# Kernel tuning notes

Measured on AMD Instinct MI355X. Metric: run time of the kernel, lower is better.

## Reference

```python
import jax, jax.numpy as jnp
import numpy as np

N, MAX_NB, H, L, V, B, M = 16384, 15, 512, 128, 1024, 256, 65536


def setup_inputs() -> dict:
    key = jax.random.key(0)
    ks = jax.random.split(key, 32)
    s = 0.02  # param init scale
    inp = {
        'x_ids': jax.random.randint(ks[0], (N,), 0, V, dtype=jnp.int32),
        'contexts': jax.random.randint(ks[1], (N,), 0, B, dtype=jnp.int32),
        'nei_idx': jax.random.randint(ks[2], (N, MAX_NB), 0, M, dtype=jnp.int32),
        'nei_mask': jax.random.randint(ks[3], (N, MAX_NB), 0, 2, dtype=jnp.int32),
        'o_idx': jax.random.randint(ks[4], (N, MAX_NB), 0, M, dtype=jnp.int32),
        'o_mask': jax.random.randint(ks[5], (N, MAX_NB), 0, 2, dtype=jnp.int32),
        'H_msg': jax.random.normal(ks[6], (M, H), jnp.float32),
        'x_tree_vecs': jax.random.normal(ks[7], (B, L), jnp.float32),
        'embedding': jax.random.normal(ks[8], (V, H), jnp.float32) * s,
        'Wz_w': jax.random.normal(ks[9], (H, 2 * H), jnp.float32) * s,
        'Wz_b': jnp.zeros((H,), jnp.float32),
        'Wr_w': jax.random.normal(ks[10], (H, H), jnp.float32) * s,
        'Wr_b': jnp.zeros((H,), jnp.float32),
        'Ur_w': jax.random.normal(ks[11], (H, H), jnp.float32) * s,
        'Wh_w': jax.random.normal(ks[12], (H, 2 * H), jnp.float32) * s,
        'Wh_b': jnp.zeros((H,), jnp.float32),
        'W_w': jax.random.normal(ks[13], (H, H + L), jnp.float32) * s,
        'W_b': jnp.zeros((H,), jnp.float32),
        'Wo_w': jax.random.normal(ks[14], (V, H), jnp.float32) * s,
        'Wo_b': jnp.zeros((V,), jnp.float32),
        'Ui_w': jax.random.normal(ks[15], (H, 2 * H), jnp.float32) * s,
        'Ui_b': jnp.zeros((H,), jnp.float32),
        'U_w': jax.random.normal(ks[16], (H, H + L), jnp.float32) * s,
        'U_b': jnp.zeros((H,), jnp.float32),
        'Uo_w': jax.random.normal(ks[17], (1, H), jnp.float32) * s,
        'Uo_b': jnp.zeros((1,), jnp.float32),
    }
    return inp


def _gru(x, h_nei, Wz_w, Wz_b, Wr_w, Wr_b, Ur_w, Wh_w, Wh_b):
    # x: [N,H], h_nei: [N,MAX_NB,H]
    sum_h = h_nei.sum(axis=1)
    z = jax.nn.sigmoid(jnp.concatenate([x, sum_h], axis=1) @ Wz_w.T + Wz_b)
    r1 = (x @ Wr_w.T + Wr_b)[:, None, :]          # [N,1,H]
    r2 = jnp.einsum('nkh,gh->nkg', h_nei, Ur_w)   # U_r(h_nei), no bias
    r = jax.nn.sigmoid(r1 + r2)
    sum_gated = (r * h_nei).sum(axis=1)
    pre_h = jnp.tanh(jnp.concatenate([x, sum_gated], axis=1) @ Wh_w.T + Wh_b)
    return (1.0 - z) * sum_h + z * pre_h


def reference(x_ids, contexts, nei_idx, nei_mask, o_idx, o_mask, H_msg,
              x_tree_vecs, embedding, Wz_w, Wz_b, Wr_w, Wr_b, Ur_w,
              Wh_w, Wh_b, W_w, W_b, Wo_w, Wo_b, Ui_w, Ui_b, U_w, U_b,
              Uo_w, Uo_b):
    x = embedding[x_ids]                                   # [N,H]
    h_nei = H_msg[nei_idx] * nei_mask[..., None].astype(H_msg.dtype)  # [N,NB,H]
    o_nei = H_msg[o_idx] * o_mask[..., None].astype(H_msg.dtype)
    new_h = _gru(x, h_nei, Wz_w, Wz_b, Wr_w, Wr_b, Ur_w, Wh_w, Wh_b)
    cur_o = o_nei.sum(axis=1)                              # [N,H]
    ctx = x_tree_vecs[contexts]                            # [N,L]
    # word prediction: aggregate(new_h, contexts, x_tree_vecs, 'word')
    w_hid = jax.nn.relu(jnp.concatenate([new_h, ctx], axis=1) @ W_w.T + W_b)
    word_scores = w_hid @ Wo_w.T + Wo_b                    # [N,V]
    # stop prediction: U_i(cat(x, cur_o)) -> aggregate(..., 'stop')
    stop_h = jax.nn.relu(jnp.concatenate([x, cur_o], axis=1) @ Ui_w.T + Ui_b)
    s_hid = jax.nn.relu(jnp.concatenate([stop_h, ctx], axis=1) @ U_w.T + U_b)
    stop_scores = s_hid @ Uo_w.T + Uo_b                    # [N,1]
    return jnp.concatenate([word_scores, stop_scores], axis=1)  # [N,V+1]
```

## Files before the change

kernel.cpp:

```cpp
#include <hip/hip_runtime.h>
#include <hip/hip_bf16.h>

typedef unsigned short u16;
typedef unsigned int u32;
typedef __attribute__((ext_vector_type(8))) short s8v;
typedef __attribute__((ext_vector_type(4))) float f4v;

#define HDIM 512
#define NNODE 16384
#define NB 15

__device__ __forceinline__ u16 f2bu(float x) {
  union { float f; u32 i; } v; v.f = x;
  u32 r = v.i + 0x7FFFu + ((v.i >> 16) & 1u);
  return (u16)(r >> 16);
}
__device__ __forceinline__ float bu2f(u16 u) {
  union { u32 i; float f; } v; v.i = ((u32)u) << 16;
  return v.f;
}
__device__ __forceinline__ u32 pk(float a, float b) {
  return (u32)f2bu(a) | ((u32)f2bu(b) << 16);
}
__device__ __forceinline__ float sigm(float x) {
  return __builtin_amdgcn_rcpf(1.f + __expf(-x));
}
__device__ __forceinline__ void gl16(const void* g, void* l) {
  __builtin_amdgcn_global_load_lds(
      (const __attribute__((address_space(1))) u32*)g,
      (__attribute__((address_space(3))) u32*)l, 16, 0, 0);
}
template<int N> __device__ __forceinline__ void wait_vm() {
  if constexpr (N == 0) asm volatile("s_waitcnt vmcnt(0)" ::: "memory");
  else if constexpr (N == 2) asm volatile("s_waitcnt vmcnt(2)" ::: "memory");
  else asm volatile("s_waitcnt vmcnt(4)" ::: "memory");
}

__global__ __launch_bounds__(256) void k_cvt_all(
    const float* Wz_w, const float* Wr_w, const float* Wh_w, const float* Ui_w,
    const float* Ur_w, const float* W_w, const float* U_w, const float* Wo_w,
    const float* emb, const float* xtree,
    const float* Wz_b, const float* Wr_b, const float* Wh_b, const float* Ui_b,
    const float* W_b, const float* U_b,
    u16* wcat, u16* wz_h, u16* wh_h, u16* ui_h, u16* ur, u16* w_n, u16* u_n,
    u16* ccat, u16* wo, u16* emb_bf, u16* xt_bf, float* ebias, float* cbias) {
  int seg = blockIdx.y;
  const float* src = nullptr; u16* dst = nullptr;
  const float* fsrc = nullptr; float* fdst = nullptr;
  int R = 0, Cs = 0, c0 = 0, C = 0, fn = 0;
  switch (seg) {
    case 0:  src = Wz_w; dst = wcat;              R = 512;  Cs = 1024; c0 = 0;   C = 512; break;
    case 1:  src = Wr_w; dst = wcat + 512 * 512;  R = 512;  Cs = 512;  c0 = 0;   C = 512; break;
    case 2:  src = Wh_w; dst = wcat + 1024 * 512; R = 512;  Cs = 1024; c0 = 0;   C = 512; break;
    case 3:  src = Ui_w; dst = wcat + 1536 * 512; R = 512;  Cs = 1024; c0 = 0;   C = 512; break;
    case 4:  src = Wz_w; dst = wz_h;              R = 512;  Cs = 1024; c0 = 512; C = 512; break;
    case 5:  src = Wh_w; dst = wh_h;              R = 512;  Cs = 1024; c0 = 512; C = 512; break;
    case 6:  src = Ui_w; dst = ui_h;              R = 512;  Cs = 1024; c0 = 512; C = 512; break;
    case 7:  src = Ur_w; dst = ur;                R = 512;  Cs = 512;  c0 = 0;   C = 512; break;
    case 8:  src = W_w;  dst = w_n;               R = 512;  Cs = 640;  c0 = 0;   C = 512; break;
    case 9:  src = U_w;  dst = u_n;               R = 512;  Cs = 640;  c0 = 0;   C = 512; break;
    case 10: src = W_w;  dst = ccat;              R = 512;  Cs = 640;  c0 = 512; C = 128; break;
    case 11: src = U_w;  dst = ccat + 512 * 128;  R = 512;  Cs = 640;  c0 = 512; C = 128; break;
    case 12: src = Wo_w; dst = wo;                R = 1024; Cs = 512;  c0 = 0;   C = 512; break;
    case 13: src = emb;  dst = emb_bf;            R = 1024; Cs = 512;  c0 = 0;   C = 512; break;
    case 14: src = xtree; dst = xt_bf;            R = 256;  Cs = 128;  c0 = 0;   C = 128; break;
    case 15: fsrc = Wz_b; fdst = ebias;        fn = 512; break;
    case 16: fsrc = Wr_b; fdst = ebias + 512;  fn = 512; break;
    case 17: fsrc = Wh_b; fdst = ebias + 1024; fn = 512; break;
    case 18: fsrc = Ui_b; fdst = ebias + 1536; fn = 512; break;
    case 19: fsrc = W_b;  fdst = cbias;        fn = 512; break;
    case 20: fsrc = U_b;  fdst = cbias + 512;  fn = 512; break;
  }
  int i = blockIdx.x * 256 + threadIdx.x;
  if (fdst) { if (i < fn) fdst[i] = fsrc[i]; return; }
  int e0 = i * 8;
  if (e0 >= R * C) return;
  int r = e0 / C, c = e0 - r * C;
  const float* s = src + (size_t)r * Cs + c0 + c;
  float4 a = *reinterpret_cast<const float4*>(s);
  float4 b = *reinterpret_cast<const float4*>(s + 4);
  uint4 o = {pk(a.x, a.y), pk(a.z, a.w), pk(b.x, b.y), pk(b.z, b.w)};
  *reinterpret_cast<uint4*>(&dst[e0]) = o;
}

__global__ void k_cvtH(const float* __restrict__ src, u16* __restrict__ HR) {
  size_t i = ((size_t)blockIdx.x * 256 + threadIdx.x) * 8;
  size_t m = i >> 9, c = i & 511;
  float4 a = *reinterpret_cast<const float4*>(src + i);
  float4 b = *reinterpret_cast<const float4*>(src + i + 4);
  uint4 o = {pk(a.x, a.y), pk(a.z, a.w), pk(b.x, b.y), pk(b.z, b.w)};
  *reinterpret_cast<uint4*>(&HR[m * 1024 + c]) = o;
}

struct GP {
  const u16* A; const u16* B; int K; int lda;
  const float* gadd; int ldg; const int* gidx;
  const float* bias; const u16* shb;
  float* outf; u16* outh; int ldo;
};

template<int EP>
__device__ __forceinline__ void epi(int row, int col, float v, const GP& g) {
  if constexpr (EP == 0) {
    g.outf[(size_t)row * g.ldo + col] = v + (g.bias ? g.bias[col] : 0.f);
  } else if constexpr (EP == 3) {
    float pre = v + g.gadd[(size_t)g.gidx[row] * g.ldg + col];
    g.outh[(size_t)row * g.ldo + col] = f2bu(pre > 0.f ? pre : 0.f);
  } else {
    g.outh[(size_t)row * g.ldo + col] = f2bu(v);
  }
}

template<int EP, int KV>
__device__ void gemm_core(const GP& g, u16* AsB, u16* BsB) {
  const int tid = threadIdx.x, lane = tid & 63, w = tid >> 6;
  const int wm = (w >> 2) * 64, wn = (w & 3) * 32;
  const int nx = gridDim.x;
  int orig = blockIdx.y * nx + blockIdx.x;
  int q = (nx * gridDim.y) >> 3;
  int tile = (orig & 7) * q + (orig >> 3);
  const int n0 = (tile % nx) * 128, m0 = (tile / nx) * 128;

  const int sr = tid >> 2, sc = (tid & 3) ^ (sr & 3);
  const u16* gA = g.A + (size_t)(m0 + sr) * g.lda + sc * 8;
  const u16* gB = g.B + (size_t)(n0 + sr) * KV + sc * 8;
  const int ls = tid * 8;

  f4v acc[4][2];
  f4v z4 = {0.f, 0.f, 0.f, 0.f};
#pragma unroll
  for (int a = 0; a < 4; a++) { acc[a][0] = z4; acc[a][1] = z4; }

  constexpr int T = KV / 32;
  auto STAGE = [&](int t) {
    int buf = (t & 3) * 4096;
    gl16(gA + t * 32, AsB + buf + ls);
    gl16(gB + t * 32, BsB + buf + ls);
  };
  STAGE(0); STAGE(1); STAGE(2);

#pragma unroll
  for (int t = 0; t < T; t++) {
    if (t < T - 2) wait_vm<4>();
    else if (t == T - 2) wait_vm<2>();
    else wait_vm<0>();
    __builtin_amdgcn_s_barrier();
    asm volatile("" ::: "memory");
    if (t + 3 < T) STAGE(t + 3);
    const u16* as = AsB + (t & 3) * 4096;
    const u16* bs = BsB + (t & 3) * 4096;
    s8v af[4], bf[2];
    int cc = lane >> 4;
#pragma unroll
    for (int i = 0; i < 4; i++) {
      int R = wm + i * 16 + (lane & 15);
      af[i] = *reinterpret_cast<const s8v*>(&as[R * 32 + (cc ^ (R & 3)) * 8]);
    }
#pragma unroll
    for (int i = 0; i < 2; i++) {
      int C = wn + i * 16 + (lane & 15);
      bf[i] = *reinterpret_cast<const s8v*>(&bs[C * 32 + (cc ^ (C & 3)) * 8]);
    }
#pragma unroll
    for (int mi = 0; mi < 4; mi++)
#pragma unroll
      for (int ni = 0; ni < 2; ni++)
        acc[mi][ni] = __builtin_amdgcn_mfma_f32_16x16x32_bf16(
            af[mi], bf[ni], acc[mi][ni], 0, 0, 0);
  }
#pragma unroll
  for (int mi = 0; mi < 4; mi++)
#pragma unroll
    for (int ni = 0; ni < 2; ni++)
#pragma unroll
      for (int r = 0; r < 4; r++) {
        int row = m0 + wm + mi * 16 + (lane >> 4) * 4 + r;
        int col = n0 + wn + ni * 16 + (lane & 15);
        epi<EP>(row, col, acc[mi][ni][r], g);
      }
}

template<int EP, int KV>
__global__ __launch_bounds__(512, 4) void k_gemm(GP g) {
  __shared__ u16 As[4 * 4096], Bs[4 * 4096];
  gemm_core<EP, KV>(g, As, Bs);
}

template<int EPa, int EPb, int KV>
__global__ __launch_bounds__(512, 4) void k_pair(GP a, GP b) {
  __shared__ u16 As[4 * 4096], Bs[4 * 4096];
  if (blockIdx.z == 0) gemm_core<EPa, KV>(a, As, Bs);
  else gemm_core<EPb, KV>(b, As, Bs);
}

__global__ __launch_bounds__(512, 4) void k_zn(
    const u16* __restrict__ sumh, const u16* __restrict__ sg,
    const u16* __restrict__ Wz, const u16* __restrict__ Wh,
    const float* __restrict__ E_z, const float* __restrict__ E_h, int ldg,
    const int* __restrict__ gidx, u16* __restrict__ newh) {
  __shared__ u16 As1[128 * 64], Bs1[128 * 64], As2[128 * 64], Bs2[128 * 64];
  const int tid = threadIdx.x, lane = tid & 63, w = tid >> 6;
  const int wm = (w >> 2) * 64, wn = (w & 3) * 32;
  const int nx = gridDim.x;
  int orig = blockIdx.y * nx + blockIdx.x;
  int q = (nx * gridDim.y) >> 3;
  int tile = (orig & 7) * q + (orig >> 3);
  const int n0 = (tile % nx) * 128, m0 = (tile / nx) * 128;

  const u16 *gA1[2], *gA2[2], *gB1[2], *gB2[2]; int ls[2];
#pragma unroll
  for (int i = 0; i < 2; i++) {
    int slot = tid + i * 512;
    int r = slot >> 3, c = (slot & 7) ^ (r & 7);
    gA1[i] = sumh + (size_t)(m0 + r) * HDIM + c * 8;
    gA2[i] = sg + (size_t)(m0 + r) * HDIM + c * 8;
    gB1[i] = Wz + (size_t)(n0 + r) * HDIM + c * 8;
    gB2[i] = Wh + (size_t)(n0 + r) * HDIM + c * 8;
    ls[i] = slot * 8;
  }

  f4v az[4][2], ah[4][2];
  f4v z4 = {0.f, 0.f, 0.f, 0.f};
#pragma unroll
  for (int a = 0; a < 4; a++) {
    az[a][0] = z4; az[a][1] = z4; ah[a][0] = z4; ah[a][1] = z4;
  }

  for (int k0 = 0; k0 < HDIM; k0 += 64) {
    __syncthreads();
#pragma unroll
    for (int i = 0; i < 2; i++) gl16(gA1[i] + k0, As1 + ls[i]);
#pragma unroll
    for (int i = 0; i < 2; i++) gl16(gB1[i] + k0, Bs1 + ls[i]);
#pragma unroll
    for (int i = 0; i < 2; i++) gl16(gA2[i] + k0, As2 + ls[i]);
#pragma unroll
    for (int i = 0; i < 2; i++) gl16(gB2[i] + k0, Bs2 + ls[i]);
    __syncthreads();
#pragma unroll
    for (int ks = 0; ks < 2; ks++) {
      int cc = ks * 4 + (lane >> 4);
      {
        s8v af[4], bf[2];
#pragma unroll
        for (int i = 0; i < 4; i++) {
          int R = wm + i * 16 + (lane & 15);
          af[i] = *reinterpret_cast<const s8v*>(&As1[R * 64 + (cc ^ (R & 7)) * 8]);
        }
#pragma unroll
        for (int i = 0; i < 2; i++) {
          int C = wn + i * 16 + (lane & 15);
          bf[i] = *reinterpret_cast<const s8v*>(&Bs1[C * 64 + (cc ^ (C & 7)) * 8]);
        }
#pragma unroll
        for (int mi = 0; mi < 4; mi++)
#pragma unroll
          for (int ni = 0; ni < 2; ni++)
            az[mi][ni] = __builtin_amdgcn_mfma_f32_16x16x32_bf16(
                af[mi], bf[ni], az[mi][ni], 0, 0, 0);
      }
      {
        s8v af[4], bf[2];
#pragma unroll
        for (int i = 0; i < 4; i++) {
          int R = wm + i * 16 + (lane & 15);
          af[i] = *reinterpret_cast<const s8v*>(&As2[R * 64 + (cc ^ (R & 7)) * 8]);
        }
#pragma unroll
        for (int i = 0; i < 2; i++) {
          int C = wn + i * 16 + (lane & 15);
          bf[i] = *reinterpret_cast<const s8v*>(&Bs2[C * 64 + (cc ^ (C & 7)) * 8]);
        }
#pragma unroll
        for (int mi = 0; mi < 4; mi++)
#pragma unroll
          for (int ni = 0; ni < 2; ni++)
            ah[mi][ni] = __builtin_amdgcn_mfma_f32_16x16x32_bf16(
                af[mi], bf[ni], ah[mi][ni], 0, 0, 0);
      }
    }
  }
#pragma unroll
  for (int mi = 0; mi < 4; mi++)
#pragma unroll
    for (int r = 0; r < 4; r++) {
      int row = m0 + wm + mi * 16 + (lane >> 4) * 4 + r;
      int xid = gidx[row];
      const float* ez = E_z + (size_t)xid * ldg;
      const float* eh = E_h + (size_t)xid * ldg;
#pragma unroll
      for (int ni = 0; ni < 2; ni++) {
        int col = n0 + wn + ni * 16 + (lane & 15);
        float zv = sigm(az[mi][ni][r] + ez[col]);
        float pre = tanhf(ah[mi][ni][r] + eh[col]);
        float sh = bu2f(sumh[(size_t)row * HDIM + col]);
        newh[(size_t)row * HDIM + col] = f2bu((1.f - zv) * sh + zv * pre);
      }
    }
}

__global__ __launch_bounds__(256) void k_gsr(
    const u16* __restrict__ HR,
    const float* __restrict__ E_r, int ldg, const int* __restrict__ x_ids,
    const int* __restrict__ nei_idx, const int* __restrict__ nei_mask,
    const int* __restrict__ o_idx, const int* __restrict__ o_mask,
    u16* __restrict__ sum_h_bf, u16* __restrict__ sg_bf,
    u16* __restrict__ cur_o_bf) {
  int t = threadIdx.x;
  int nd = t >> 7, lt = t & 127;
  int n = blockIdx.x * 2 + nd;
  __shared__ int sidx[2][NB], smsk[2][NB], soid[2][NB], somk[2][NB];
  __shared__ int sx[2];
  if (lt < NB) {
    sidx[nd][lt] = nei_idx[(size_t)n * NB + lt];
    smsk[nd][lt] = nei_mask[(size_t)n * NB + lt];
  } else if (lt >= 32 && lt < 32 + NB) {
    int k = lt - 32;
    soid[nd][k] = o_idx[(size_t)n * NB + k];
    somk[nd][k] = o_mask[(size_t)n * NB + k];
  } else if (lt == 64) {
    sx[nd] = x_ids[n];
  }
  __syncthreads();
  int c = lt * 4;
  float4 e = *reinterpret_cast<const float4*>(E_r + (size_t)sx[nd] * ldg + c);
  float s0 = 0.f, s1 = 0.f, s2 = 0.f, s3 = 0.f;
  float g0 = 0.f, g1 = 0.f, g2 = 0.f, g3 = 0.f;
  float o0 = 0.f, o1 = 0.f, o2 = 0.f, o3 = 0.f;
#pragma unroll
  for (int k = 0; k < NB; k++) {
    if (smsk[nd][k]) {
      const u16* row = HR + (size_t)sidx[nd][k] * 1024;
      uint2 hv = *reinterpret_cast<const uint2*>(row + c);
      uint2 rv = *reinterpret_cast<const uint2*>(row + 512 + c);
      float h0 = bu2f((u16)hv.x), h1 = bu2f((u16)(hv.x >> 16));
      float h2 = bu2f((u16)hv.y), h3 = bu2f((u16)(hv.y >> 16));
      s0 += h0; s1 += h1; s2 += h2; s3 += h3;
      g0 += sigm(bu2f((u16)rv.x) + e.x) * h0;
      g1 += sigm(bu2f((u16)(rv.x >> 16)) + e.y) * h1;
      g2 += sigm(bu2f((u16)rv.y) + e.z) * h2;
      g3 += sigm(bu2f((u16)(rv.y >> 16)) + e.w) * h3;
    }
    if (somk[nd][k]) {
      uint2 ov = *reinterpret_cast<const uint2*>(HR + (size_t)soid[nd][k] * 1024 + c);
      o0 += bu2f((u16)ov.x); o1 += bu2f((u16)(ov.x >> 16));
      o2 += bu2f((u16)ov.y); o3 += bu2f((u16)(ov.y >> 16));
    }
  }
  size_t b = (size_t)n * HDIM + c;
  uint2 ps = {pk(s0, s1), pk(s2, s3)};
  uint2 pg = {pk(g0, g1), pk(g2, g3)};
  uint2 po = {pk(o0, o1), pk(o2, o3)};
  *reinterpret_cast<uint2*>(&sum_h_bf[b]) = ps;
  *reinterpret_cast<uint2*>(&sg_bf[b]) = pg;
  *reinterpret_cast<uint2*>(&cur_o_bf[b]) = po;
}

__global__ __launch_bounds__(256) void k_stop(
    const u16* __restrict__ shid, const float* __restrict__ Uo_w,
    const float* __restrict__ Uo_b, float* __restrict__ out) {
  int n = blockIdx.x * 4 + (threadIdx.x >> 6);
  int lane = threadIdx.x & 63;
  float s = 0.f;
  for (int j = lane; j < HDIM; j += 64)
    s += bu2f(shid[(size_t)n * HDIM + j]) * Uo_w[j];
#pragma unroll
  for (int off = 32; off; off >>= 1) s += __shfl_xor(s, off, 64);
  if (lane == 0) out[(size_t)n * 1025 + 1024] = s + Uo_b[0];
}

extern "C" void kernel_launch(void* const* d_in, const int* in_sizes, int n_in,
                              void* d_out, int out_size, void* d_ws, size_t ws_size,
                              hipStream_t stream) {
  const int* x_ids = (const int*)d_in[0];
  const int* contexts = (const int*)d_in[1];
  const int* nei_idx = (const int*)d_in[2];
  const int* nei_mask = (const int*)d_in[3];
  const int* o_idx = (const int*)d_in[4];
  const int* o_mask = (const int*)d_in[5];
  const float* H_msg = (const float*)d_in[6];
  const float* xtree = (const float*)d_in[7];
  const float* emb = (const float*)d_in[8];
  const float* Wz_w = (const float*)d_in[9];  const float* Wz_b = (const float*)d_in[10];
  const float* Wr_w = (const float*)d_in[11]; const float* Wr_b = (const float*)d_in[12];
  const float* Ur_w = (const float*)d_in[13];
  const float* Wh_w = (const float*)d_in[14]; const float* Wh_b = (const float*)d_in[15];
  const float* W_w  = (const float*)d_in[16]; const float* W_b  = (const float*)d_in[17];
  const float* Wo_w = (const float*)d_in[18]; const float* Wo_b = (const float*)d_in[19];
  const float* Ui_w = (const float*)d_in[20]; const float* Ui_b = (const float*)d_in[21];
  const float* U_w  = (const float*)d_in[22]; const float* U_b  = (const float*)d_in[23];
  const float* Uo_w = (const float*)d_in[24]; const float* Uo_b = (const float*)d_in[25];
  float* out = (float*)d_out;
  const int M = 65536;

  char* base = (char*)d_ws;
  size_t ofs = 0;
  auto alloc = [&](size_t bytes) -> char* {
    char* p = base + ofs;
    ofs = (ofs + bytes + 255) & ~(size_t)255;
    return p;
  };
  u16* wcat  = (u16*)alloc((size_t)2048 * 512 * 2);
  u16* wz_h  = (u16*)alloc(512 * 512 * 2);
  u16* wh_h  = (u16*)alloc(512 * 512 * 2);
  u16* ui_h  = (u16*)alloc(512 * 512 * 2);
  u16* ur    = (u16*)alloc(512 * 512 * 2);
  u16* w_n   = (u16*)alloc(512 * 512 * 2);
  u16* u_n   = (u16*)alloc(512 * 512 * 2);
  u16* ccat  = (u16*)alloc(1024 * 128 * 2);
  u16* wo    = (u16*)alloc(1024 * 512 * 2);
  u16* emb_bf = (u16*)alloc(1024 * 512 * 2);
  u16* xt_bf  = (u16*)alloc(256 * 128 * 2);
  float* ebias = (float*)alloc(2048 * 4);
  float* cbias = (float*)alloc(1024 * 4);
  float* E_cat = (float*)alloc((size_t)1024 * 2048 * 4);
  float* C_cat = (float*)alloc((size_t)256 * 1024 * 4);
  u16* HR = (u16*)alloc((size_t)M * 1024 * 2);
  u16* sum_h_bf = (u16*)alloc((size_t)NNODE * HDIM * 2);
  u16* cur_o_bf = (u16*)alloc((size_t)NNODE * HDIM * 2);
  u16* sg_bf    = (u16*)alloc((size_t)NNODE * HDIM * 2);
  u16* newh_bf  = (u16*)alloc((size_t)NNODE * HDIM * 2);
  u16* whid_bf  = (u16*)alloc((size_t)NNODE * HDIM * 2);
  u16* stoph_bf = (u16*)alloc((size_t)NNODE * HDIM * 2);
  u16* shid_bf  = (u16*)alloc((size_t)NNODE * HDIM * 2);

  k_cvt_all<<<dim3(256, 21), dim3(256), 0, stream>>>(
      Wz_w, Wr_w, Wh_w, Ui_w, Ur_w, W_w, U_w, Wo_w, emb, xtree,
      Wz_b, Wr_b, Wh_b, Ui_b, W_b, U_b,
      wcat, wz_h, wh_h, ui_h, ur, w_n, u_n, ccat, wo, emb_bf, xt_bf,
      ebias, cbias);
  k_cvtH<<<dim3(16384), dim3(256), 0, stream>>>(H_msg, HR);

  GP ge{emb_bf, wcat, 512, 512, nullptr, 0, nullptr, ebias, nullptr,
        E_cat, nullptr, 2048};
  k_gemm<0, 512><<<dim3(16, 8), dim3(512), 0, stream>>>(ge);
  GP gc{xt_bf, ccat, 128, 128, nullptr, 0, nullptr, cbias, nullptr,
        C_cat, nullptr, 1024};
  k_gemm<0, 128><<<dim3(8, 2), dim3(512), 0, stream>>>(gc);

  GP gr{HR, ur, 512, 1024, nullptr, 0, nullptr, nullptr, nullptr,
        nullptr, HR + 512, 1024};
  k_gemm<4, 512><<<dim3(4, 512), dim3(512), 0, stream>>>(gr);

  k_gsr<<<dim3(NNODE / 2), dim3(256), 0, stream>>>(
      HR, E_cat + 512, 2048, x_ids, nei_idx, nei_mask, o_idx, o_mask,
      sum_h_bf, sg_bf, cur_o_bf);

  GP gs{cur_o_bf, ui_h, 512, 512, E_cat + 1536, 2048, x_ids, nullptr, nullptr,
        nullptr, stoph_bf, 512};
  k_gemm<3, 512><<<dim3(4, 128), dim3(512), 0, stream>>>(gs);

  k_zn<<<dim3(4, 128), dim3(512), 0, stream>>>(
      sum_h_bf, sg_bf, wz_h, wh_h, E_cat, E_cat + 1024, 2048, x_ids, newh_bf);

  GP gw{newh_bf, w_n, 512, 512, C_cat, 1024, contexts, nullptr, nullptr,
        nullptr, whid_bf, 512};
  GP gu{stoph_bf, u_n, 512, 512, C_cat + 512, 1024, contexts, nullptr, nullptr,
        nullptr, shid_bf, 512};
  k_pair<3, 3, 512><<<dim3(4, 128, 2), dim3(512), 0, stream>>>(gw, gu);

  GP gword{whid_bf, wo, 512, 512, nullptr, 0, nullptr, Wo_b, nullptr,
           out, nullptr, 1025};
  k_gemm<0, 512><<<dim3(8, 128), dim3(512), 0, stream>>>(gword);

  k_stop<<<dim3(NNODE / 4), dim3(256), 0, stream>>>(shid_bf, Uo_w, Uo_b, out);
}
```

Baseline: 331.8 us.

## Fuse stop GEMM into z/n kernel, merge stop head into word GEMM, widen gather

Merges the stop-hidden GEMM into the GRU z/n kernel via a z-dimension split, and folds the stop-score dot product into the word-score GEMM launch, removing two kernel launches and their tail effects. The neighbour-gather kernel now handles four nodes per block with 16-byte loads per lane. MFMA loops get s_setprio raises so compute waves are favoured over memory waves. Sharing one grid means the two merged halves have different work per block, which could cause load imbalance.

```diff
diff --git a/kernel.cpp b/kernel.cpp
--- a/kernel.cpp
+++ b/kernel.cpp
@@ -161,12 +161,14 @@
       int C = wn + i * 16 + (lane & 15);
       bf[i] = *reinterpret_cast<const s8v*>(&bs[C * 32 + (cc ^ (C & 3)) * 8]);
     }
+    __builtin_amdgcn_s_setprio(1);
 #pragma unroll
     for (int mi = 0; mi < 4; mi++)
 #pragma unroll
       for (int ni = 0; ni < 2; ni++)
         acc[mi][ni] = __builtin_amdgcn_mfma_f32_16x16x32_bf16(
             af[mi], bf[ni], acc[mi][ni], 0, 0, 0);
+    __builtin_amdgcn_s_setprio(0);
   }
 #pragma unroll
   for (int mi = 0; mi < 4; mi++)
@@ -193,12 +195,15 @@
   else gemm_core<EPb, KV>(b, As, Bs);
 }
 
-__global__ __launch_bounds__(512, 4) void k_zn(
+__global__ __launch_bounds__(512, 4) void k_znp(
     const u16* __restrict__ sumh, const u16* __restrict__ sg,
     const u16* __restrict__ Wz, const u16* __restrict__ Wh,
     const float* __restrict__ E_z, const float* __restrict__ E_h, int ldg,
-    const int* __restrict__ gidx, u16* __restrict__ newh) {
-  __shared__ u16 As1[128 * 64], Bs1[128 * 64], As2[128 * 64], Bs2[128 * 64];
+    const int* __restrict__ gidx, u16* __restrict__ newh, GP gs) {
+  __shared__ u16 S[32768];
+  if (blockIdx.z == 1) { gemm_core<3, 512>(gs, S, S + 16384); return; }
+  u16* As1 = S; u16* Bs1 = S + 8192;
+  u16* As2 = S + 16384; u16* Bs2 = S + 24576;
   const int tid = threadIdx.x, lane = tid & 63, w = tid >> 6;
   const int wm = (w >> 2) * 64, wn = (w & 3) * 32;
   const int nx = gridDim.x;
@@ -252,12 +257,14 @@
           int C = wn + i * 16 + (lane & 15);
           bf[i] = *reinterpret_cast<const s8v*>(&Bs1[C * 64 + (cc ^ (C & 7)) * 8]);
         }
+        __builtin_amdgcn_s_setprio(1);
 #pragma unroll
         for (int mi = 0; mi < 4; mi++)
 #pragma unroll
           for (int ni = 0; ni < 2; ni++)
             az[mi][ni] = __builtin_amdgcn_mfma_f32_16x16x32_bf16(
                 af[mi], bf[ni], az[mi][ni], 0, 0, 0);
+        __builtin_amdgcn_s_setprio(0);
       }
       {
         s8v af[4], bf[2];
@@ -271,12 +278,14 @@
           int C = wn + i * 16 + (lane & 15);
           bf[i] = *reinterpret_cast<const s8v*>(&Bs2[C * 64 + (cc ^ (C & 7)) * 8]);
         }
+        __builtin_amdgcn_s_setprio(1);
 #pragma unroll
         for (int mi = 0; mi < 4; mi++)
 #pragma unroll
           for (int ni = 0; ni < 2; ni++)
             ah[mi][ni] = __builtin_amdgcn_mfma_f32_16x16x32_bf16(
                 af[mi], bf[ni], ah[mi][ni], 0, 0, 0);
+        __builtin_amdgcn_s_setprio(0);
       }
     }
   }
@@ -307,66 +316,92 @@
     u16* __restrict__ sum_h_bf, u16* __restrict__ sg_bf,
     u16* __restrict__ cur_o_bf) {
   int t = threadIdx.x;
-  int nd = t >> 7, lt = t & 127;
-  int n = blockIdx.x * 2 + nd;
-  __shared__ int sidx[2][NB], smsk[2][NB], soid[2][NB], somk[2][NB];
-  __shared__ int sx[2];
-  if (lt < NB) {
-    sidx[nd][lt] = nei_idx[(size_t)n * NB + lt];
-    smsk[nd][lt] = nei_mask[(size_t)n * NB + lt];
-  } else if (lt >= 32 && lt < 32 + NB) {
-    int k = lt - 32;
-    soid[nd][k] = o_idx[(size_t)n * NB + k];
-    somk[nd][k] = o_mask[(size_t)n * NB + k];
-  } else if (lt == 64) {
-    sx[nd] = x_ids[n];
+  int nd = t >> 6, lane = t & 63;
+  int n = blockIdx.x * 4 + nd;
+  __shared__ int sidx[4][NB], smsk[4][NB], soid[4][NB], somk[4][NB];
+  __shared__ int sx[4];
+  if (t < 60) {
+    int nn = t / 15, k = t - nn * 15;
+    size_t gofs = (size_t)(blockIdx.x * 4 + nn) * NB + k;
+    sidx[nn][k] = nei_idx[gofs];
+    smsk[nn][k] = nei_mask[gofs];
+  } else if (t >= 64 && t < 124) {
+    int tt = t - 64;
+    int nn = tt / 15, k = tt - nn * 15;
+    size_t gofs = (size_t)(blockIdx.x * 4 + nn) * NB + k;
+    soid[nn][k] = o_idx[gofs];
+    somk[nn][k] = o_mask[gofs];
+  } else if (t >= 128 && t < 132) {
+    sx[t - 128] = x_ids[blockIdx.x * 4 + (t - 128)];
   }
   __syncthreads();
-  int c = lt * 4;
-  float4 e = *reinterpret_cast<const float4*>(E_r + (size_t)sx[nd] * ldg + c);
-  float s0 = 0.f, s1 = 0.f, s2 = 0.f, s3 = 0.f;
-  float g0 = 0.f, g1 = 0.f, g2 = 0.f, g3 = 0.f;
-  float o0 = 0.f, o1 = 0.f, o2 = 0.f, o3 = 0.f;
+  int c = lane * 8;
+  const float* er = E_r + (size_t)sx[nd] * ldg + c;
+  float4 e0 = *reinterpret_cast<const float4*>(er);
+  float4 e1 = *reinterpret_cast<const float4*>(er + 4);
+  float ev[8] = {e0.x, e0.y, e0.z, e0.w, e1.x, e1.y, e1.z, e1.w};
+  float s[8], gg[8], oo[8];
+#pragma unroll
+  for (int i = 0; i < 8; i++) { s[i] = 0.f; gg[i] = 0.f; oo[i] = 0.f; }
 #pragma unroll
   for (int k = 0; k < NB; k++) {
     if (smsk[nd][k]) {
-      const u16* row = HR + (size_t)sidx[nd][k] * 1024;
-      uint2 hv = *reinterpret_cast<const uint2*>(row + c);
-      uint2 rv = *reinterpret_cast<const uint2*>(row + 512 + c);
-      float h0 = bu2f((u16)hv.x), h1 = bu2f((u16)(hv.x >> 16));
-      float h2 = bu2f((u16)hv.y), h3 = bu2f((u16)(hv.y >> 16));
-      s0 += h0; s1 += h1; s2 += h2; s3 += h3;
-      g0 += sigm(bu2f((u16)rv.x) + e.x) * h0;
-      g1 += sigm(bu2f((u16)(rv.x >> 16)) + e.y) * h1;
-      g2 += sigm(bu2f((u16)rv.y) + e.z) * h2;
-      g3 += sigm(bu2f((u16)(rv.y >> 16)) + e.w) * h3;
+      const u16* row = HR + (size_t)sidx[nd][k] * 1024 + c;
+      uint4 hv = *reinterpret_cast<const uint4*>(row);
+      uint4 rv = *reinterpret_cast<const uint4*>(row + 512);
+      u32 ha[4] = {hv.x, hv.y, hv.z, hv.w};
+      u32 ra[4] = {rv.x, rv.y, rv.z, rv.w};
+#pragma unroll
+      for (int p = 0; p < 4; p++) {
+        float h0 = bu2f((u16)ha[p]), h1 = bu2f((u16)(ha[p] >> 16));
+        s[p * 2] += h0; s[p * 2 + 1] += h1;
+        gg[p * 2] += sigm(bu2f((u16)ra[p]) + ev[p * 2]) * h0;
+        gg[p * 2 + 1] += sigm(bu2f((u16)(ra[p] >> 16)) + ev[p * 2 + 1]) * h1;
+      }
     }
     if (somk[nd][k]) {
-      uint2 ov = *reinterpret_cast<const uint2*>(HR + (size_t)soid[nd][k] * 1024 + c);
-      o0 += bu2f((u16)ov.x); o1 += bu2f((u16)(ov.x >> 16));
-      o2 += bu2f((u16)ov.y); o3 += bu2f((u16)(ov.y >> 16));
+      uint4 ov = *reinterpret_cast<const uint4*>(
+          HR + (size_t)soid[nd][k] * 1024 + c);
+      u32 oa[4] = {ov.x, ov.y, ov.z, ov.w};
+#pragma unroll
+      for (int p = 0; p < 4; p++) {
+        oo[p * 2] += bu2f((u16)oa[p]);
+        oo[p * 2 + 1] += bu2f((u16)(oa[p] >> 16));
+      }
     }
   }
   size_t b = (size_t)n * HDIM + c;
-  uint2 ps = {pk(s0, s1), pk(s2, s3)};
-  uint2 pg = {pk(g0, g1), pk(g2, g3)};
-  uint2 po = {pk(o0, o1), pk(o2, o3)};
-  *reinterpret_cast<uint2*>(&sum_h_bf[b]) = ps;
-  *reinterpret_cast<uint2*>(&sg_bf[b]) = pg;
-  *reinterpret_cast<uint2*>(&cur_o_bf[b]) = po;
-}
-
-__global__ __launch_bounds__(256) void k_stop(
-    const u16* __restrict__ shid, const float* __restrict__ Uo_w,
+  uint4 ps = {pk(s[0], s[1]), pk(s[2], s[3]), pk(s[4], s[5]), pk(s[6], s[7])};
+  uint4 pg = {pk(gg[0], gg[1]), pk(gg[2], gg[3]), pk(gg[4], gg[5]), pk(gg[6], gg[7])};
+  uint4 po = {pk(oo[0], oo[1]), pk(oo[2], oo[3]), pk(oo[4], oo[5]), pk(oo[6], oo[7])};
+  *reinterpret_cast<uint4*>(&sum_h_bf[b]) = ps;
+  *reinterpret_cast<uint4*>(&sg_bf[b]) = pg;
+  *reinterpret_cast<uint4*>(&cur_o_bf[b]) = po;
+}
+
+__global__ __launch_bounds__(512, 4) void k_wordstop(
+    GP wgp, const u16* __restrict__ shid, const float* __restrict__ Uo_w,
     const float* __restrict__ Uo_b, float* __restrict__ out) {
-  int n = blockIdx.x * 4 + (threadIdx.x >> 6);
-  int lane = threadIdx.x & 63;
-  float s = 0.f;
-  for (int j = lane; j < HDIM; j += 64)
-    s += bu2f(shid[(size_t)n * HDIM + j]) * Uo_w[j];
-#pragma unroll
-  for (int off = 32; off; off >>= 1) s += __shfl_xor(s, off, 64);
-  if (lane == 0) out[(size_t)n * 1025 + 1024] = s + Uo_b[0];
+  __shared__ u16 As[4 * 4096], Bs[4 * 4096];
+  if (blockIdx.z == 0) { gemm_core<0, 512>(wgp, As, Bs); return; }
+  int b = blockIdx.y * gridDim.x + blockIdx.x;
+  int wv = threadIdx.x >> 6, lane = threadIdx.x & 63;
+#pragma unroll
+  for (int i = 0; i < 2; i++) {
+    int n = b * 16 + wv * 2 + i;
+    const u16* row = shid + (size_t)n * HDIM + lane * 8;
+    const float* uw = Uo_w + lane * 8;
+    uint4 v = *reinterpret_cast<const uint4*>(row);
+    float4 u0 = *reinterpret_cast<const float4*>(uw);
+    float4 u1 = *reinterpret_cast<const float4*>(uw + 4);
+    float s = bu2f((u16)v.x) * u0.x + bu2f((u16)(v.x >> 16)) * u0.y +
+              bu2f((u16)v.y) * u0.z + bu2f((u16)(v.y >> 16)) * u0.w +
+              bu2f((u16)v.z) * u1.x + bu2f((u16)(v.z >> 16)) * u1.y +
+              bu2f((u16)v.w) * u1.z + bu2f((u16)(v.w >> 16)) * u1.w;
+#pragma unroll
+    for (int off = 32; off; off >>= 1) s += __shfl_xor(s, off, 64);
+    if (lane == 0) out[(size_t)n * 1025 + 1024] = s + Uo_b[0];
+  }
 }
 
 extern "C" void kernel_launch(void* const* d_in, const int* in_sizes, int n_in,
@@ -442,16 +477,15 @@
         nullptr, HR + 512, 1024};
   k_gemm<4, 512><<<dim3(4, 512), dim3(512), 0, stream>>>(gr);
 
-  k_gsr<<<dim3(NNODE / 2), dim3(256), 0, stream>>>(
+  k_gsr<<<dim3(NNODE / 4), dim3(256), 0, stream>>>(
       HR, E_cat + 512, 2048, x_ids, nei_idx, nei_mask, o_idx, o_mask,
       sum_h_bf, sg_bf, cur_o_bf);
 
   GP gs{cur_o_bf, ui_h, 512, 512, E_cat + 1536, 2048, x_ids, nullptr, nullptr,
         nullptr, stoph_bf, 512};
-  k_gemm<3, 512><<<dim3(4, 128), dim3(512), 0, stream>>>(gs);
-
-  k_zn<<<dim3(4, 128), dim3(512), 0, stream>>>(
-      sum_h_bf, sg_bf, wz_h, wh_h, E_cat, E_cat + 1024, 2048, x_ids, newh_bf);
+  k_znp<<<dim3(4, 128, 2), dim3(512), 0, stream>>>(
+      sum_h_bf, sg_bf, wz_h, wh_h, E_cat, E_cat + 1024, 2048, x_ids,
+      newh_bf, gs);
 
   GP gw{newh_bf, w_n, 512, 512, C_cat, 1024, contexts, nullptr, nullptr,
         nullptr, whid_bf, 512};
@@ -461,7 +495,6 @@
 
   GP gword{whid_bf, wo, 512, 512, nullptr, 0, nullptr, Wo_b, nullptr,
            out, nullptr, 1025};
-  k_gemm<0, 512><<<dim3(8, 128), dim3(512), 0, stream>>>(gword);
-
-  k_stop<<<dim3(NNODE / 4), dim3(256), 0, stream>>>(shid_bf, Uo_w, Uo_b, out);
-}
+  k_wordstop<<<dim3(8, 128, 2), dim3(512), 0, stream>>>(
+      gword, shid_bf, Uo_w, Uo_b, out);
+}
```

New measurement: 320.1 us. -3.5%, faster.
